# Optimization experiments

Hardware: AMD Instinct MI355X
Metric: run time of the kernel (lower is better)

Reference implementation:

```python
import jax, jax.numpy as jnp
import numpy as np
from jax import lax

# 16 overlapping 4x4 patches of the 7x7 board, grouped by which of the 3 shared
# conv stacks processes them: (y0, y1, x0, x1, rot90_k, transpose)
CHUNKS = [
    [(0, 4, 0, 4, 0, False), (0, 4, 3, 7, 1, False), (3, 7, 3, 7, 2, False), (3, 7, 0, 4, 3, False)],
    [(0, 4, 1, 5, 0, False), (1, 5, 3, 7, 1, False), (3, 7, 2, 6, 2, False), (2, 6, 0, 4, 3, False),
     (1, 5, 0, 4, 0, True), (0, 4, 2, 6, 1, True), (2, 6, 3, 7, 2, True), (3, 7, 1, 5, 3, True)],
    [(1, 5, 1, 5, 0, False), (1, 5, 2, 6, 1, False), (2, 6, 2, 6, 2, False), (2, 6, 1, 5, 3, False)],
]
QMAX = 127.0 / 128.0


def fake_quant(x, scale=128.0, num_bits=8):
    qmin = -(2.0 ** (num_bits - 1))
    qmax = 2.0 ** (num_bits - 1) - 1.0
    q = jnp.clip(jnp.round(x * scale), qmin, qmax) / scale
    return x + lax.stop_gradient(q - x)  # straight-through estimator


def conv2d(x, w, b):
    y = lax.conv_general_dilated(x, w, (1, 1), 'VALID',
                                 dimension_numbers=('NCHW', 'OIHW', 'NCHW'))
    return y + b[None, :, None, None]


def bn(x, p, eps=1e-5):
    # p: [4, C] = (gamma, beta, running_mean, running_var), eval-mode BN
    g, be, m, v = p[0], p[1], p[2], p[3]
    inv = g * lax.rsqrt(v + eps)
    return (x - m[None, :, None, None]) * inv[None, :, None, None] + be[None, :, None, None]


def mapping_stack(x, W, B, BN):
    # W/B: 6 conv weights/biases; BN: 5 bn params for layers 1..5
    x = jax.nn.relu(conv2d(x, W[0], B[0]))
    for i in range(1, 5):
        x = jax.nn.relu(bn(conv2d(x, W[i], B[i]), BN[i - 1]))
    x = bn(conv2d(x, W[5], B[5]), BN[4])  # -> [N, 32, 1, 1]
    return x


def qlinear(x, w, b, in_scale=128.0, w_scale=128.0, w_bits=8, b_bits=32):
    xq = fake_quant(x, in_scale)
    wq = fake_quant(w, w_scale, w_bits)
    bq = fake_quant(b, in_scale * w_scale, b_bits)
    return xq @ wq.T + bq


def setup_inputs() -> dict:
    key = jax.random.key(0)
    ks = iter(jax.random.split(key, 64))
    DM, DF, CIN = 128, 32, 2
    d = {}
    d['x'] = jax.random.normal(next(ks), (16384, CIN, 7, 7), dtype=jnp.float32)
    # conv stack params, stacked over the 3 mapping groups
    shapes_w = [(DM, CIN, 2, 2), (DM, DM, 1, 1), (DM, DM, 2, 2), (DM, DM, 1, 1), (DM, DM, 2, 2), (DF, DM, 1, 1)]
    for i, s in enumerate(shapes_w):
        fan_in = s[1] * s[2] * s[3]
        d[f'w{i}'] = jax.random.normal(next(ks), (3,) + s, dtype=jnp.float32) / np.sqrt(fan_in)
        d[f'b{i}'] = jax.random.normal(next(ks), (3, s[0]), dtype=jnp.float32) * 0.05
    for i in range(1, 6):
        C = shapes_w[i][0]
        g = 1.0 + 0.1 * jax.random.normal(next(ks), (3, C), dtype=jnp.float32)
        be = 0.05 * jax.random.normal(next(ks), (3, C), dtype=jnp.float32)
        m = 0.1 * jax.random.normal(next(ks), (3, C), dtype=jnp.float32)
        v = 0.5 + jax.random.uniform(next(ks), (3, C), dtype=jnp.float32)
        d[f'bn{i}'] = jnp.stack([g, be, m, v], axis=1)  # [3, 4, C]
    # quantized value MLP: 32 -> 32 -> 32 -> 3
    for i, (o, ii) in enumerate([(32, DF), (32, 32), (3, 32)]):
        d[f'vw{i}'] = jax.random.normal(next(ks), (o, ii), dtype=jnp.float32) / np.sqrt(ii)
        d[f'vb{i}'] = jax.random.normal(next(ks), (o,), dtype=jnp.float32) * 0.05
    return d


def reference(x, w0, b0, w1, b1, w2, b2, w3, b3, w4, b4, w5, b5,
              bn1, bn2, bn3, bn4, bn5, vw0, vb0, vw1, vb1, vw2, vb2):
    B = x.shape[0]
    Ws = [w0, w1, w2, w3, w4, w5]
    Bs = [b0, b1, b2, b3, b4, b5]
    BNs = [bn1, bn2, bn3, bn4, bn5]
    feats_all = []
    for g, chunk_list in enumerate(CHUNKS):
        chunks = []
        for (y0, y1, x0, x1, k, t) in chunk_list:
            c = jnp.rot90(x[:, :, y0:y1, x0:x1], k, axes=(2, 3))
            if t:
                c = jnp.swapaxes(c, 2, 3)
            chunks.append(c)
        cb = jnp.concatenate(chunks, axis=0)  # [n_chunks*B, 2, 4, 4]
        f = mapping_stack(cb, [w[g] for w in Ws], [b[g] for b in Bs], [p[g] for p in BNs])
        f = f[:, :, 0, 0].reshape(len(chunk_list), B, -1)  # [n_chunks, B, 32]
        feats_all.append(jnp.clip(f, -1.0, QMAX))
    feature = jnp.sum(fake_quant(jnp.concatenate(feats_all, axis=0), 128.0), axis=0)  # [B, 32]
    v = jnp.clip(feature, -1.0, QMAX)
    v = qlinear(v, vw0, vb0, w_scale=256.0)
    v = jnp.clip(v, 0.0, QMAX)
    v = qlinear(v, vw1, vb1)
    v = jnp.clip(v, 0.0, QMAX)
    v = qlinear(v, vw2, vb2)  # [B, 3]
    policy = jnp.zeros((B, 7, 7), dtype=feature.dtype)
    return (v, policy)
```

## Files before the change

### kernel.cpp

```cpp
#include <hip/hip_runtime.h>
#include <stdint.h>


typedef _Float16 f16x8 __attribute__((ext_vector_type(8)));
typedef _Float16 f16x4 __attribute__((ext_vector_type(4)));
typedef float f32x4 __attribute__((ext_vector_type(4)));

static __device__ __constant__ int CH_Y0[16] = {0,0,3,3, 0,1,3,2, 1,0,2,3, 1,1,2,2};
static __device__ __constant__ int CH_X0[16] = {0,3,3,0, 1,3,2,0, 0,2,3,1, 1,2,2,1};
static __device__ __constant__ int CH_K [16] = {0,1,2,3, 0,1,2,3, 0,1,2,3, 0,1,2,3};
static __device__ __constant__ int CH_T [16] = {0,0,0,0, 0,0,0,0, 1,1,1,1, 0,0,0,0};

#define G_STRIDE 678912
#define GW1   0
#define GW2   65536
#define GW3   327680
#define GW4   393216
#define GW5   655360
#define GW0   671744
#define GBIAS 675840
#define G_WORDS   167936
#define G_STRIDE_W 169728
#define MLP_WORD_OFF 509184
#define FEAT_OFF_BYTES (2*1024*1024)

#define LO_SCALE 2048.0f
#define LO_INV   (1.0f/2048.0f)

__device__ __forceinline__ int base3(int z){ return (z>>1)*3 + (z&1); }
__device__ __forceinline__ int clampi(int v, int lo, int hi) { return v < lo ? lo : (v > hi ? hi : v); }
__device__ __forceinline__ int f0swz(int row){ return (row ^ (row>>2)) & 7; }

__device__ inline float bninv(const float* bn, int g, int C, int c) {
  float ga = bn[(g*4+0)*C + c];
  float va = bn[(g*4+3)*C + c];
  return ga / sqrtf(va + 1e-5f);
}
__device__ inline int q8(float x) { return clampi((int)rintf(x), -128, 127); }

__global__ void prep_kernel(
    const float* __restrict__ w0, const float* __restrict__ b0,
    const float* __restrict__ w1, const float* __restrict__ b1,
    const float* __restrict__ w2, const float* __restrict__ b2,
    const float* __restrict__ w3, const float* __restrict__ b3,
    const float* __restrict__ w4, const float* __restrict__ b4,
    const float* __restrict__ w5, const float* __restrict__ b5,
    const float* __restrict__ bn1, const float* __restrict__ bn2,
    const float* __restrict__ bn3, const float* __restrict__ bn4,
    const float* __restrict__ bn5,
    const float* __restrict__ vw0, const float* __restrict__ vb0,
    const float* __restrict__ vw1, const float* __restrict__ vb1,
    const float* __restrict__ vw2, const float* __restrict__ vb2,
    float* __restrict__ ws)
{
  int idx = blockIdx.x * blockDim.x + threadIdx.x;
  if (idx < 3*G_WORDS) {
    uint32_t* wsU = (uint32_t*)ws;
    int g = idx / G_WORDS;
    int q = idx - g*G_WORDS;
    int stage, blk = 0, sub;
    if      (q < 16384)  { stage = 1; sub = q; }
    else if (q < 81920)  { stage = 2; blk = (q-16384)>>14; sub = (q-16384)&16383; }
    else if (q < 98304)  { stage = 3; sub = q-81920; }
    else if (q < 163840) { stage = 4; blk = (q-98304)>>14; sub = (q-98304)&16383; }
    else                 { stage = 5; sub = q-163840; }
    int isLo, r;
    if (stage == 5) { isLo = sub>>11; r = sub&2047; }
    else            { isLo = sub>>13; r = sub&8191; }
    int pb = r*4;
    int lb = pb ^ (((pb>>8)&7)<<4);
    int oc = lb>>8;
    int k0 = (lb&255)>>1;
    float inv, v0, v1;
    if (stage == 1) {
      inv = bninv(bn1,g,128,oc);
      v0 = w1[(g*128+oc)*128+k0]; v1 = w1[(g*128+oc)*128+k0+1];
    } else if (stage == 2) {
      inv = bninv(bn2,g,128,oc);
      v0 = w2[((g*128+oc)*128+k0)*4+blk]; v1 = w2[((g*128+oc)*128+k0+1)*4+blk];
    } else if (stage == 3) {
      inv = bninv(bn3,g,128,oc);
      v0 = w3[(g*128+oc)*128+k0]; v1 = w3[(g*128+oc)*128+k0+1];
    } else if (stage == 4) {
      inv = bninv(bn4,g,128,oc);
      v0 = w4[((g*128+oc)*128+k0)*4+blk]; v1 = w4[((g*128+oc)*128+k0+1)*4+blk];
    } else {
      inv = bninv(bn5,g,32,oc);
      v0 = w5[(g*32+oc)*128+k0]; v1 = w5[(g*32+oc)*128+k0+1];
    }
    v0 *= inv; v1 *= inv;
    _Float16 h0 = (_Float16)v0, h1 = (_Float16)v1;
    if (isLo) {
      h0 = (_Float16)((v0 - (float)h0) * LO_SCALE);
      h1 = (_Float16)((v1 - (float)h1) * LO_SCALE);
    }
    union { _Float16 h[2]; uint32_t u; } uu;
    uu.h[0] = h0; uu.h[1] = h1;
    wsU[g*G_STRIDE_W + q] = uu.u;
  } else if (idx < 506880) {
    int e = idx - 503808; int g = e>>10; int t2 = e&1023;
    int k = t2>>7, c = t2&127;
    ws[g*G_STRIDE_W + 167936 + t2] = w0[((g*128 + c)*2 + (k>>2))*4 + (k&3)];
  } else if (idx < 509184) {
    int e = idx - 506880; int g = e/768; int r = e - g*768;
    int l = r>>7, c = r&127;
    float t;
    if (l == 0) {
      t = b0[g*128 + c];
    } else if (l < 5) {
      const float* bn = (l==1) ? bn1 : (l==2) ? bn2 : (l==3) ? bn3 : bn4;
      const float* bb = (l==1) ? b1  : (l==2) ? b2  : (l==3) ? b3  : b4;
      float inv = bninv(bn, g, 128, c);
      t = (bb[g*128 + c] - bn[(g*4+2)*128 + c]) * inv + bn[(g*4+1)*128 + c];
    } else {
      if (c < 32) {
        float inv = bninv(bn5, g, 32, c);
        t = (b5[g*32 + c] - bn5[(g*4+2)*32 + c]) * inv + bn5[(g*4+1)*32 + c];
      } else t = 0.f;
    }
    ws[g*G_STRIDE_W + 168960 + r] = t;
  } else if (idx < 511395) {
    int e = idx - MLP_WORD_OFF;
    int* wsI = (int*)ws;
    int val;
    if      (e < 1024) val = q8(vw0[e] * 256.f);
    else if (e < 1056) val = (int)rintf(vb0[e-1024] * 32768.f);
    else if (e < 2080) val = q8(vw1[e-1056] * 128.f);
    else if (e < 2112) val = (int)rintf(vb1[e-2080] * 16384.f);
    else if (e < 2208) val = q8(vw2[e-2112] * 128.f);
    else               val = (int)rintf(vb2[e-2208] * 16384.f);
    wsI[idx] = val;
  }
}

#define MFMA(a,b,c) __builtin_amdgcn_mfma_f32_16x16x32_f16((a),(b),(c),0,0,0)

template<int MT, int NT, int MODE>
__device__ __forceinline__ void phaseF(const char* AHb, const char* ALb,
    const char* __restrict__ gwH,
    int m0, int n0, int lane, int blk, f32x4 acc1[][NT], f32x4 acc2[][NT])
{
  const int l15 = lane & 15, kq = (lane >> 4) & 3;
#pragma unroll
  for (int kb = 0; kb < 4; ++kb) {
    const int ko2 = (kb*32 + kq*8)*2;
    f16x8 Bh_[NT];
#pragma unroll
    for (int n = 0; n < NT; ++n) {
      int brow = (n0+n)*16 + l15;
      int boff = (brow*256 + ko2) ^ ((brow&7)<<4);
      Bh_[n] = *(const f16x8*)(gwH + boff);
    }
#pragma unroll
    for (int m = 0; m < MT; ++m) {
      const int rr = (m0+m)*16 + l15;
      int row, f;
      if (MODE == 0)      { row = rr; f = f0swz(rr); }
      else if (MODE == 2) { int s = rr>>2; int w = base3(rr&3) + base3(blk);
                            row = s*9 + w; f = ((s&3)<<1) | (w&1); }
      else                { row = rr*4 + blk; f = rr & 7; }
      const int aoff = (row*256 + ko2) ^ (f<<4);
      f16x8 Ah = *(const f16x8*)(AHb + aoff);
      f16x8 Al = *(const f16x8*)(ALb + aoff);
#pragma unroll
      for (int n = 0; n < NT; ++n) {
        acc1[m][n] = MFMA(Ah, Bh_[n], acc1[m][n]);
        acc2[m][n] = MFMA(Al, Bh_[n], acc2[m][n]);
      }
    }
  }
}

template<int GEN>
__device__ __forceinline__ void wbvalG(char* ah, char* al, int row, int col, float v) {
  _Float16 h = (_Float16)v;
  _Float16 l = (_Float16)((v - (float)h) * LO_SCALE);
  int f;
  if (GEN == 0)      f = f0swz(row);
  else if (GEN == 2) { int s = (row*57)>>9; int w = row - s*9; f = ((s&3)<<1) | (w&1); }
  else               f = (row >> 2) & 7;
  int sb = (row*256 + col*2) ^ (f<<4);
  *(_Float16*)(ah + sb) = h;
  *(_Float16*)(al + sb) = l;
}

template<int MT, int NT, int GEN>
__device__ __forceinline__ void writeback(char* AHb, char* ALb,
    const float* __restrict__ biasG,
    int layer, int m0, int n0, int lane, f32x4 acc1[][NT], f32x4 acc2[][NT])
{
  const int l15 = lane & 15, rq = (lane >> 4) & 3;
#pragma unroll
  for (int m = 0; m < MT; ++m)
#pragma unroll
    for (int n = 0; n < NT; ++n) {
      int col = (n0+n)*16 + l15;
      float bb = biasG[layer*128 + col];
#pragma unroll
      for (int q = 0; q < 4; ++q) {
        int row = (m0+m)*16 + rq*4 + q;
        float v = acc1[m][n][q] + acc2[m][n][q]*LO_INV + bb;
        v = fmaxf(v, 0.f);
        wbvalG<GEN>(AHb, ALb, row, col, v);
      }
    }
}

__global__ __launch_bounds__(256, 2)
void conv_mfma(
    const float* __restrict__ x, const char* __restrict__ wsb,
    signed char* __restrict__ feat, int B, int wgPerChunk)
{
  __shared__ __align__(16) char ldsbuf[73728];
  char* AHb = ldsbuf;
  char* ALb = ldsbuf + 36864;

  const int tid  = threadIdx.x;
  const int lane = tid & 63;
  const int wave = tid >> 6;

  const int wg = blockIdx.x;
  const int chunkG = wg / wgPerChunk;
  const int b0 = (wg - chunkG*wgPerChunk) * 16;
  const int g = (chunkG < 4) ? 0 : (chunkG < 12) ? 1 : 2;
  const char* gw = wsb + g*G_STRIDE;
  const float* biasG = (const float*)(gw + GBIAS);

  {
    const int s0 = tid >> 5, u = tid & 31;
    const int ic = u >> 4, pos = u & 15;
    const int i = pos >> 2, j2 = pos & 3;
    int tt = CH_T[chunkG], kk = CH_K[chunkG];
    int a = tt ? j2 : i, bb2 = tt ? i : j2;
    int py, px;
    if      (kk == 0) { py = a;     px = bb2;   }
    else if (kk == 1) { py = bb2;   px = 3-a;   }
    else if (kk == 2) { py = 3-a;   px = 3-bb2; }
    else              { py = 3-bb2; px = a;     }
    int sy = CH_Y0[chunkG] + py, sx = CH_X0[chunkG] + px;
    const float* w0s = (const float*)(gw + GW0);
    float4 wr[8];
#pragma unroll
    for (int k = 0; k < 8; ++k) wr[k] = ((const float4*)(w0s + k*128))[u];
    float4 bb4 = ((const float4*)biasG)[u];
    float bbv[4] = {bb4.x, bb4.y, bb4.z, bb4.w};
    const int gbase = lane & 32;
#pragma unroll
    for (int p = 0; p < 2; ++p) {
      int sp = s0 + p*8;
      float xval = x[((b0+sp)*2 + ic)*49 + sy*7 + sx];
      float xv[32];
#pragma unroll
      for (int t2 = 0; t2 < 32; ++t2) xv[t2] = __shfl(xval, gbase | t2, 64);
#pragma unroll
      for (int oy = 0; oy < 3; ++oy)
#pragma unroll
        for (int ox = 0; ox < 3; ++ox) {
          float accv[4];
#pragma unroll
          for (int q = 0; q < 4; ++q) accv[q] = bbv[q];
#pragma unroll
          for (int ic2 = 0; ic2 < 2; ++ic2)
#pragma unroll
            for (int dy = 0; dy < 2; ++dy)
#pragma unroll
              for (int dx = 0; dx < 2; ++dx) {
                float xvv = xv[ic2*16 + (oy+dy)*4 + ox+dx];
                int k = ic2*4 + dy*2 + dx;
                accv[0] = fmaf(xvv, wr[k].x, accv[0]);
                accv[1] = fmaf(xvv, wr[k].y, accv[1]);
                accv[2] = fmaf(xvv, wr[k].z, accv[2]);
                accv[3] = fmaf(xvv, wr[k].w, accv[3]);
              }
          int row = sp*9 + oy*3 + ox;
          f16x4 hv, lv;
#pragma unroll
          for (int q = 0; q < 4; ++q) {
            float v = fmaxf(accv[q], 0.f);
            _Float16 h = (_Float16)v;
            hv[q] = h;
            lv[q] = (_Float16)((v - (float)h) * LO_SCALE);
          }
          int sb = (row*256 + u*8) ^ (f0swz(row)<<4);
          *(f16x4*)(AHb + sb) = hv;
          *(f16x4*)(ALb + sb) = lv;
        }
    }
  }
  __syncthreads();

  {
    {
      f32x4 a1[2][4] = {}; f32x4 a2[2][4] = {};
      phaseF<2,4,0>(AHb, ALb, gw+GW1, (wave>>1)*2, (wave&1)*4, lane, 0, a1, a2);
      __syncthreads();
      writeback<2,4,2>(AHb, ALb, biasG, 1, (wave>>1)*2, (wave&1)*4, lane, a1, a2);
    }
    {
      f32x4 a1[2][4] = {}; f32x4 a2[2][4] = {};
      phaseF<2,4,0>(AHb, ALb, gw+GW1, 4+(wave>>1)*2, (wave&1)*4, lane, 0, a1, a2);
      __syncthreads();
      writeback<2,4,2>(AHb, ALb, biasG, 1, 4+(wave>>1)*2, (wave&1)*4, lane, a1, a2);
    }
    {
      f32x4 a1[1][2] = {}; f32x4 a2[1][2] = {};
      phaseF<1,2,0>(AHb, ALb, gw+GW1, 8, wave*2, lane, 0, a1, a2);
      __syncthreads();
      writeback<1,2,2>(AHb, ALb, biasG, 1, 8, wave*2, lane, a1, a2);
    }
  }
  __syncthreads();

  {
    f32x4 a1[2][4] = {}; f32x4 a2[2][4] = {};
#pragma unroll
    for (int blk = 0; blk < 4; ++blk)
      phaseF<2,4,2>(AHb, ALb, gw+GW2+blk*65536,
                    (wave>>1)*2, (wave&1)*4, lane, blk, a1, a2);
    __syncthreads();
    writeback<2,4,0>(AHb, ALb, biasG, 2, (wave>>1)*2, (wave&1)*4, lane, a1, a2);
  }
  __syncthreads();

  {
    f32x4 a1[2][4] = {}; f32x4 a2[2][4] = {};
    phaseF<2,4,0>(AHb, ALb, gw+GW3, (wave>>1)*2, (wave&1)*4, lane, 0, a1, a2);
    __syncthreads();
    writeback<2,4,4>(AHb, ALb, biasG, 3, (wave>>1)*2, (wave&1)*4, lane, a1, a2);
  }
  __syncthreads();

  {
    f32x4 a1[1][2] = {}; f32x4 a2[1][2] = {};
#pragma unroll
    for (int blk = 0; blk < 4; ++blk)
      phaseF<1,2,4>(AHb, ALb, gw+GW4+blk*65536,
                    0, wave*2, lane, blk, a1, a2);
    __syncthreads();
    writeback<1,2,0>(AHb, ALb, biasG, 4, 0, wave*2, lane, a1, a2);
  }
  __syncthreads();

  if (wave < 2) {
    f32x4 a1[1][1] = {}; f32x4 a2[1][1] = {};
    phaseF<1,1,0>(AHb, ALb, gw+GW5, 0, wave, lane, 0, a1, a2);
    int c = wave*16 + (lane & 15);
    float bb = biasG[5*128 + c];
#pragma unroll
    for (int q = 0; q < 4; ++q) {
      int s = ((lane >> 4) & 3)*4 + q;
      float f = a1[0][0][q] + a2[0][0][q]*LO_INV + bb;
      f = fminf(fmaxf(f, -1.0f), 127.0f/128.0f);
      int qi = clampi((int)rintf(f * 128.0f), -128, 127);
      feat[((long)chunkG*B + b0 + s)*32 + c] = (signed char)qi;
    }
  }
}

__global__ __launch_bounds__(256) void mlp_kernel(
    const signed char* __restrict__ feat,
    const int* __restrict__ mw,
    float* __restrict__ out, int B)
{
  int b = blockIdx.x * blockDim.x + threadIdx.x;
  if (b >= B) return;
  int S[32];
#pragma unroll
  for (int c = 0; c < 32; ++c) S[c] = 0;
  for (int ch = 0; ch < 16; ++ch) {
    const signed char* f = feat + ((long)ch*B + b)*32;
#pragma unroll
    for (int c = 0; c < 32; ++c) S[c] += f[c];
  }
  int x1[32];
#pragma unroll
  for (int c = 0; c < 32; ++c) x1[c] = clampi(S[c], -128, 127);

  const int* wq0 = mw;        const int* bq0 = mw + 1024;
  const int* wq1 = mw + 1056; const int* bq1 = mw + 2080;
  const int* wq2 = mw + 2112; const int* bq2 = mw + 2208;

  int x2[32];
#pragma unroll
  for (int o = 0; o < 32; ++o) {
    int acc = bq0[o];
    for (int i = 0; i < 32; ++i) acc += x1[i] * wq0[o*32 + i];
    acc = clampi(acc, 0, 32512);
    int r = acc >> 8, fr = acc & 255;
    r += (fr > 128 || (fr == 128 && (r & 1))) ? 1 : 0;
    x2[o] = r;
  }
  int x3[32];
#pragma unroll
  for (int o = 0; o < 32; ++o) {
    int acc = bq1[o];
    for (int i = 0; i < 32; ++i) acc += x2[i] * wq1[o*32 + i];
    acc = clampi(acc, 0, 16256);
    int r = acc >> 7, fr = acc & 127;
    r += (fr > 64 || (fr == 64 && (r & 1))) ? 1 : 0;
    x3[o] = r;
  }
  for (int o = 0; o < 3; ++o) {
    int acc = bq2[o];
    for (int i = 0; i < 32; ++i) acc += x3[i] * wq2[o*32 + i];
    out[b*3 + o] = (float)acc / 16384.0f;
  }
}

__global__ void zero_kernel(float4* __restrict__ p, int n4) {
  int i = blockIdx.x * blockDim.x + threadIdx.x;
  if (i < n4) p[i] = make_float4(0.f, 0.f, 0.f, 0.f);
}

extern "C" void kernel_launch(void* const* d_in, const int* in_sizes, int n_in,
                              void* d_out, int out_size, void* d_ws, size_t ws_size,
                              hipStream_t stream)
{
  const float* x   = (const float*)d_in[0];
  const float* w0  = (const float*)d_in[1];
  const float* b0  = (const float*)d_in[2];
  const float* w1  = (const float*)d_in[3];
  const float* b1  = (const float*)d_in[4];
  const float* w2  = (const float*)d_in[5];
  const float* b2  = (const float*)d_in[6];
  const float* w3  = (const float*)d_in[7];
  const float* b3  = (const float*)d_in[8];
  const float* w4  = (const float*)d_in[9];
  const float* b4  = (const float*)d_in[10];
  const float* w5  = (const float*)d_in[11];
  const float* b5  = (const float*)d_in[12];
  const float* bn1 = (const float*)d_in[13];
  const float* bn2 = (const float*)d_in[14];
  const float* bn3 = (const float*)d_in[15];
  const float* bn4 = (const float*)d_in[16];
  const float* bn5 = (const float*)d_in[17];
  const float* vw0 = (const float*)d_in[18];
  const float* vb0 = (const float*)d_in[19];
  const float* vw1 = (const float*)d_in[20];
  const float* vb1 = (const float*)d_in[21];
  const float* vw2 = (const float*)d_in[22];
  const float* vb2 = (const float*)d_in[23];

  const int B = in_sizes[0] / 98;
  float* ws = (float*)d_ws;
  signed char* feat = (signed char*)d_ws + FEAT_OFF_BYTES;
  float* out = (float*)d_out;

  prep_kernel<<<(511395 + 255)/256, 256, 0, stream>>>(
      w0,b0,w1,b1,w2,b2,w3,b3,w4,b4,w5,b5,
      bn1,bn2,bn3,bn4,bn5, vw0,vb0,vw1,vb1,vw2,vb2, ws);

  conv_mfma<<<B, 256, 0, stream>>>(
      x, (const char*)d_ws, feat, B, B/16);

  mlp_kernel<<<(B + 255)/256, 256, 0, stream>>>(feat, (const int*)d_ws + MLP_WORD_OFF, out, B);

  {
    int n4 = B*49/4;
    zero_kernel<<<(n4 + 255)/256, 256, 0, stream>>>((float4*)(out + 3*B), n4);
  }
}
```

Baseline: 751.7 us.

## Halve samples per workgroup to shrink LDS and raise occupancy

Each workgroup now processes 8 board samples instead of 16, which shrinks the LDS activation buffers from 72KB to 40KB and doubles the grid size. The wave-to-tile mapping of every MFMA phase is reshaped to match: layer 1 covers 5 row tiles instead of 9, and layers 2 and 3 use 2x2 tiles per wave. The goal is to fit more resident workgroups per CU and hide latency better. The cost is that each workgroup streams the full weight set for fewer samples, doubling weight traffic from L2. The final 16-row MFMA tiles are also half padding, and the feature store masks out the unused rows.

```diff
diff --git a/kernel.cpp b/kernel.cpp
--- a/kernel.cpp
+++ b/kernel.cpp
@@ -10,6 +10,8 @@
 static __device__ __constant__ int CH_X0[16] = {0,3,3,0, 1,3,2,0, 0,2,3,1, 1,2,2,1};
 static __device__ __constant__ int CH_K [16] = {0,1,2,3, 0,1,2,3, 0,1,2,3, 0,1,2,3};
 static __device__ __constant__ int CH_T [16] = {0,0,0,0, 0,0,0,0, 1,1,1,1, 0,0,0,0};
+
+#define TS 8
 
 #define G_STRIDE 678912
 #define GW1   0
@@ -211,9 +213,9 @@
     const float* __restrict__ x, const char* __restrict__ wsb,
     signed char* __restrict__ feat, int B, int wgPerChunk)
 {
-  __shared__ __align__(16) char ldsbuf[73728];
+  __shared__ __align__(16) char ldsbuf[40960];
   char* AHb = ldsbuf;
-  char* ALb = ldsbuf + 36864;
+  char* ALb = ldsbuf + 20480;
 
   const int tid  = threadIdx.x;
   const int lane = tid & 63;
@@ -221,13 +223,13 @@
 
   const int wg = blockIdx.x;
   const int chunkG = wg / wgPerChunk;
-  const int b0 = (wg - chunkG*wgPerChunk) * 16;
+  const int b0 = (wg - chunkG*wgPerChunk) * TS;
   const int g = (chunkG < 4) ? 0 : (chunkG < 12) ? 1 : 2;
   const char* gw = wsb + g*G_STRIDE;
   const float* biasG = (const float*)(gw + GBIAS);
 
   {
-    const int s0 = tid >> 5, u = tid & 31;
+    const int s = tid >> 5, u = tid & 31;
     const int ic = u >> 4, pos = u & 15;
     const int i = pos >> 2, j2 = pos & 3;
     int tt = CH_T[chunkG], kk = CH_K[chunkG];
@@ -245,88 +247,77 @@
     float4 bb4 = ((const float4*)biasG)[u];
     float bbv[4] = {bb4.x, bb4.y, bb4.z, bb4.w};
     const int gbase = lane & 32;
-#pragma unroll
-    for (int p = 0; p < 2; ++p) {
-      int sp = s0 + p*8;
-      float xval = x[((b0+sp)*2 + ic)*49 + sy*7 + sx];
-      float xv[32];
-#pragma unroll
-      for (int t2 = 0; t2 < 32; ++t2) xv[t2] = __shfl(xval, gbase | t2, 64);
-#pragma unroll
-      for (int oy = 0; oy < 3; ++oy)
-#pragma unroll
-        for (int ox = 0; ox < 3; ++ox) {
-          float accv[4];
-#pragma unroll
-          for (int q = 0; q < 4; ++q) accv[q] = bbv[q];
-#pragma unroll
-          for (int ic2 = 0; ic2 < 2; ++ic2)
-#pragma unroll
-            for (int dy = 0; dy < 2; ++dy)
-#pragma unroll
-              for (int dx = 0; dx < 2; ++dx) {
-                float xvv = xv[ic2*16 + (oy+dy)*4 + ox+dx];
-                int k = ic2*4 + dy*2 + dx;
-                accv[0] = fmaf(xvv, wr[k].x, accv[0]);
-                accv[1] = fmaf(xvv, wr[k].y, accv[1]);
-                accv[2] = fmaf(xvv, wr[k].z, accv[2]);
-                accv[3] = fmaf(xvv, wr[k].w, accv[3]);
-              }
-          int row = sp*9 + oy*3 + ox;
-          f16x4 hv, lv;
-#pragma unroll
-          for (int q = 0; q < 4; ++q) {
-            float v = fmaxf(accv[q], 0.f);
-            _Float16 h = (_Float16)v;
-            hv[q] = h;
-            lv[q] = (_Float16)((v - (float)h) * LO_SCALE);
-          }
-          int sb = (row*256 + u*8) ^ (f0swz(row)<<4);
-          *(f16x4*)(AHb + sb) = hv;
-          *(f16x4*)(ALb + sb) = lv;
+    float xval = x[((b0+s)*2 + ic)*49 + sy*7 + sx];
+    float xv[32];
+#pragma unroll
+    for (int t2 = 0; t2 < 32; ++t2) xv[t2] = __shfl(xval, gbase | t2, 64);
+#pragma unroll
+    for (int oy = 0; oy < 3; ++oy)
+#pragma unroll
+      for (int ox = 0; ox < 3; ++ox) {
+        float accv[4];
+#pragma unroll
+        for (int q = 0; q < 4; ++q) accv[q] = bbv[q];
+#pragma unroll
+        for (int ic2 = 0; ic2 < 2; ++ic2)
+#pragma unroll
+          for (int dy = 0; dy < 2; ++dy)
+#pragma unroll
+            for (int dx = 0; dx < 2; ++dx) {
+              float xvv = xv[ic2*16 + (oy+dy)*4 + ox+dx];
+              int k = ic2*4 + dy*2 + dx;
+              accv[0] = fmaf(xvv, wr[k].x, accv[0]);
+              accv[1] = fmaf(xvv, wr[k].y, accv[1]);
+              accv[2] = fmaf(xvv, wr[k].z, accv[2]);
+              accv[3] = fmaf(xvv, wr[k].w, accv[3]);
+            }
+        int row = s*9 + oy*3 + ox;
+        f16x4 hv, lv;
+#pragma unroll
+        for (int q = 0; q < 4; ++q) {
+          float v = fmaxf(accv[q], 0.f);
+          _Float16 h = (_Float16)v;
+          hv[q] = h;
+          lv[q] = (_Float16)((v - (float)h) * LO_SCALE);
         }
-    }
+        int sb = (row*256 + u*8) ^ (f0swz(row)<<4);
+        *(f16x4*)(AHb + sb) = hv;
+        *(f16x4*)(ALb + sb) = lv;
+      }
   }
   __syncthreads();
 
   {
     {
-      f32x4 a1[2][4] = {}; f32x4 a2[2][4] = {};
-      phaseF<2,4,0>(AHb, ALb, gw+GW1, (wave>>1)*2, (wave&1)*4, lane, 0, a1, a2);
+      f32x4 a1[4][2] = {}; f32x4 a2[4][2] = {};
+      phaseF<4,2,0>(AHb, ALb, gw+GW1, 0, wave*2, lane, 0, a1, a2);
       __syncthreads();
-      writeback<2,4,2>(AHb, ALb, biasG, 1, (wave>>1)*2, (wave&1)*4, lane, a1, a2);
-    }
-    {
-      f32x4 a1[2][4] = {}; f32x4 a2[2][4] = {};
-      phaseF<2,4,0>(AHb, ALb, gw+GW1, 4+(wave>>1)*2, (wave&1)*4, lane, 0, a1, a2);
-      __syncthreads();
-      writeback<2,4,2>(AHb, ALb, biasG, 1, 4+(wave>>1)*2, (wave&1)*4, lane, a1, a2);
+      writeback<4,2,2>(AHb, ALb, biasG, 1, 0, wave*2, lane, a1, a2);
     }
     {
       f32x4 a1[1][2] = {}; f32x4 a2[1][2] = {};
-      phaseF<1,2,0>(AHb, ALb, gw+GW1, 8, wave*2, lane, 0, a1, a2);
+      phaseF<1,2,0>(AHb, ALb, gw+GW1, 4, wave*2, lane, 0, a1, a2);
       __syncthreads();
-      writeback<1,2,2>(AHb, ALb, biasG, 1, 8, wave*2, lane, a1, a2);
+      writeback<1,2,2>(AHb, ALb, biasG, 1, 4, wave*2, lane, a1, a2);
     }
   }
   __syncthreads();
 
   {
-    f32x4 a1[2][4] = {}; f32x4 a2[2][4] = {};
+    f32x4 a1[2][2] = {}; f32x4 a2[2][2] = {};
 #pragma unroll
     for (int blk = 0; blk < 4; ++blk)
-      phaseF<2,4,2>(AHb, ALb, gw+GW2+blk*65536,
-                    (wave>>1)*2, (wave&1)*4, lane, blk, a1, a2);
+      phaseF<2,2,2>(AHb, ALb, gw+GW2+blk*65536, 0, wave*2, lane, blk, a1, a2);
     __syncthreads();
-    writeback<2,4,0>(AHb, ALb, biasG, 2, (wave>>1)*2, (wave&1)*4, lane, a1, a2);
+    writeback<2,2,0>(AHb, ALb, biasG, 2, 0, wave*2, lane, a1, a2);
   }
   __syncthreads();
 
   {
-    f32x4 a1[2][4] = {}; f32x4 a2[2][4] = {};
-    phaseF<2,4,0>(AHb, ALb, gw+GW3, (wave>>1)*2, (wave&1)*4, lane, 0, a1, a2);
+    f32x4 a1[2][2] = {}; f32x4 a2[2][2] = {};
+    phaseF<2,2,0>(AHb, ALb, gw+GW3, 0, wave*2, lane, 0, a1, a2);
     __syncthreads();
-    writeback<2,4,4>(AHb, ALb, biasG, 3, (wave>>1)*2, (wave&1)*4, lane, a1, a2);
+    writeback<2,2,4>(AHb, ALb, biasG, 3, 0, wave*2, lane, a1, a2);
   }
   __syncthreads();
 
@@ -334,8 +325,7 @@
     f32x4 a1[1][2] = {}; f32x4 a2[1][2] = {};
 #pragma unroll
     for (int blk = 0; blk < 4; ++blk)
-      phaseF<1,2,4>(AHb, ALb, gw+GW4+blk*65536,
-                    0, wave*2, lane, blk, a1, a2);
+      phaseF<1,2,4>(AHb, ALb, gw+GW4+blk*65536, 0, wave*2, lane, blk, a1, a2);
     __syncthreads();
     writeback<1,2,0>(AHb, ALb, biasG, 4, 0, wave*2, lane, a1, a2);
   }
@@ -349,10 +339,12 @@
 #pragma unroll
     for (int q = 0; q < 4; ++q) {
       int s = ((lane >> 4) & 3)*4 + q;
-      float f = a1[0][0][q] + a2[0][0][q]*LO_INV + bb;
-      f = fminf(fmaxf(f, -1.0f), 127.0f/128.0f);
-      int qi = clampi((int)rintf(f * 128.0f), -128, 127);
-      feat[((long)chunkG*B + b0 + s)*32 + c] = (signed char)qi;
+      if (s < TS) {
+        float f = a1[0][0][q] + a2[0][0][q]*LO_INV + bb;
+        f = fminf(fmaxf(f, -1.0f), 127.0f/128.0f);
+        int qi = clampi((int)rintf(f * 128.0f), -128, 127);
+        feat[((long)chunkG*B + b0 + s)*32 + c] = (signed char)qi;
+      }
     }
   }
 }
@@ -450,8 +442,9 @@
       w0,b0,w1,b1,w2,b2,w3,b3,w4,b4,w5,b5,
       bn1,bn2,bn3,bn4,bn5, vw0,vb0,vw1,vb1,vw2,vb2, ws);
 
-  conv_mfma<<<B, 256, 0, stream>>>(
-      x, (const char*)d_ws, feat, B, B/16);
+  const int wgPerChunk = B / TS;
+  conv_mfma<<<16*wgPerChunk, 256, 0, stream>>>(
+      x, (const char*)d_ws, feat, B, wgPerChunk);
 
   mlp_kernel<<<(B + 255)/256, 256, 0, stream>>>(feat, (const int*)d_ws + MLP_WORD_OFF, out, B);
 
```

New measurement: 873.0 us. 16.1% more time.
